# Kernel optimization log

Hardware: AMD Instinct MI355X
Metric: run time of the kernel (lower is better)

## Reference

```python
import jax, jax.numpy as jnp
import numpy as np

B, S, D, C_IN = 8, 1024, 512, 7
INNER = 2 * D              # mLSTM up-projection (proj_factor=2)
NH_M, DH_M = 4, INNER // 4 # mLSTM heads = n_heads//2
NH_S, DH_S = 8, D // 8     # sLSTM heads = n_heads
K_M, K_S = 7, 4            # conv kernels: enc_in, factor
FF = int(1.1 * D)          # sLSTM gated-FFN dim (proj_factor=1.1)
EPS = 1e-6
NEG = -1e30


def _ln(x, w):
    mu = x.mean(-1, keepdims=True)
    var = x.var(-1, keepdims=True)
    return (x - mu) * jax.lax.rsqrt(var + 1e-5) * w


def _headnorm(h, w):
    # h: [B,S,NH,DH] -> per-head groupnorm -> [B,S,NH*DH] * w
    mu = h.mean(-1, keepdims=True)
    var = h.var(-1, keepdims=True)
    hn = (h - mu) * jax.lax.rsqrt(var + 1e-5)
    b, s = h.shape[:2]
    return hn.reshape(b, s, -1) * w


def _causal_conv1d(x, w, b):
    # depthwise causal conv. x: [B,S,C], w: [C,k], b: [C]
    k = w.shape[1]
    xp = jnp.pad(x, ((0, 0), (k - 1, 0), (0, 0))).transpose(0, 2, 1)  # [B,C,S+k-1]
    y = jax.lax.conv_general_dilated(
        xp, w[:, None, :], (1,), 'VALID',
        dimension_numbers=('NCH', 'OIH', 'NCH'),
        feature_group_count=w.shape[0])
    return y.transpose(0, 2, 1) + b


def _mlstm_parallel(q, k, v, i_pre, f_pre):
    # q,k,v: [B,NH,S,DH]; i_pre,f_pre: [B,NH,S]. Stabilized parallel mLSTM cell.
    s = q.shape[2]
    logf = jax.nn.log_sigmoid(f_pre)
    cum = jnp.concatenate([jnp.zeros_like(logf[:, :, :1]), jnp.cumsum(logf, -1)], -1)  # [B,NH,S+1]
    dmat = cum[:, :, 1:, None] - cum[:, :, None, 1:]            # [B,NH,S,S]
    mask = jnp.tril(jnp.ones((s, s), bool))
    dmat = jnp.where(mask, dmat, NEG) + i_pre[:, :, None, :]    # add igate along keys
    m = dmat.max(-1, keepdims=True)                              # stabilizer
    Dm = jnp.exp(dmat - m)
    qk = jnp.einsum('bhqd,bhkd->bhqk', q, k) * (q.shape[-1] ** -0.5)
    C = qk * Dm
    n = jnp.maximum(jnp.abs(C.sum(-1, keepdims=True)), jnp.exp(-m)) + EPS
    return jnp.einsum('bhqk,bhkd->bhqd', C / n, v)               # [B,NH,S,DH]


def _forward(x_enc, x_mark_enc, x_dec, x_mark_dec, W_in, b_in,
             m_ln_w, m_Wup, m_bup, m_conv_w, m_conv_b, m_Wq, m_Wk, m_Wv,
             m_Wi, m_bi, m_Wf, m_bf, m_norm_w, m_skip, m_Wdown, m_bdown,
             s_ln_w, s_conv_w, s_conv_b, s_Wi, s_Wf, s_Wz, s_Wo,
             s_Ri, s_Rf, s_Rz, s_Ro, s_bi, s_bf, s_bz, s_bo, s_norm_w,
             s_ffn_ln_w, s_Wff_up, s_bff_up, s_Wff_down, s_bff_down,
             post_norm_w, W_out, b_out):
    b, s, _ = x_enc.shape
    x = x_enc @ W_in + b_in                                    # [B,S,D]

    # ---- block 0: mLSTM block ----
    res = x
    xn = _ln(x, m_ln_w)
    xm, z = jnp.split(xn @ m_Wup + m_bup, 2, axis=-1)          # each [B,S,INNER]
    conv = jax.nn.silu(_causal_conv1d(xm, m_conv_w, m_conv_b))
    qf, kf, vf = conv @ m_Wq, conv @ m_Wk, xm @ m_Wv
    gate_in = jnp.concatenate([qf, kf, vf], -1)                # [B,S,3*INNER]
    i_pre = (gate_in @ m_Wi + m_bi).transpose(0, 2, 1)         # [B,NH,S]
    f_pre = (gate_in @ m_Wf + m_bf).transpose(0, 2, 1)
    to_h = lambda t: t.reshape(b, s, NH_M, DH_M).transpose(0, 2, 1, 3)
    h = _mlstm_parallel(to_h(qf), to_h(kf), to_h(vf), i_pre, f_pre)
    h = h.transpose(0, 2, 1, 3)                                # [B,S,NH,DH]
    h = _headnorm(h, m_norm_w) + m_skip * conv                 # learnable skip
    x = res + (h * jax.nn.silu(z)) @ m_Wdown + m_bdown

    # ---- block 1: sLSTM block + gated FFN ----
    res = x
    xn = _ln(x, s_ln_w)
    conv = jax.nn.silu(_causal_conv1d(xn, s_conv_w, s_conv_b))
    gh = lambda t: t.reshape(b, s, NH_S, DH_S).transpose(1, 0, 2, 3)  # time-major
    gi, gf = gh(conv @ s_Wi + s_bi), gh(conv @ s_Wf + s_bf)
    gz, go = gh(xn @ s_Wz + s_bz), gh(xn @ s_Wo + s_bo)

    def step(carry, xs):
        c, n, m, hp = carry
        xi, xf, xz, xo = xs
        rec = lambda R: jnp.einsum('bhd,hde->bhe', hp, R)      # block-diag recurrent
        it, ft = xi + rec(s_Ri), xf + rec(s_Rf)
        zt, ot = xz + rec(s_Rz), xo + rec(s_Ro)
        m_new = jnp.maximum(ft + m, it)                        # exp-gate stabilizer
        ig = jnp.exp(it - m_new)
        fg = jnp.exp(ft + m - m_new)
        c_new = fg * c + ig * jnp.tanh(zt)
        n_new = fg * n + ig
        h_new = jax.nn.sigmoid(ot) * c_new / jnp.maximum(n_new, EPS)
        return (c_new, n_new, m_new, h_new), h_new

    z0 = jnp.zeros((b, NH_S, DH_S), x.dtype)
    _, hs = jax.lax.scan(step, (z0, z0, z0, z0), (gi, gf, gz, go))
    x = res + _headnorm(hs.transpose(1, 0, 2, 3), s_norm_w)

    res = x
    a, g = jnp.split(_ln(x, s_ffn_ln_w) @ s_Wff_up + s_bff_up, 2, axis=-1)
    x = res + (jax.nn.gelu(a) * g) @ s_Wff_down + s_bff_down

    x = _ln(x, post_norm_w)                                    # post-blocks norm
    return x @ W_out + b_out                                   # [B,S,7]


def setup_inputs() -> dict:
    key = jax.random.key(0)
    ks = iter(jax.random.split(key, 64))
    rn = lambda shape, sc=0.02: jax.random.normal(next(ks), shape, jnp.float32) * sc
    return {
        'x_enc': jax.random.normal(next(ks), (B, S, C_IN), jnp.float32),
        'x_mark_enc': jax.random.normal(next(ks), (B, S, 4), jnp.float32),
        'x_dec': jax.random.normal(next(ks), (B, S, C_IN), jnp.float32),
        'x_mark_dec': jax.random.normal(next(ks), (B, S, 4), jnp.float32),
        'W_in': rn((C_IN, D)), 'b_in': jnp.zeros((D,)),
        'm_ln_w': jnp.ones((D,)),
        'm_Wup': rn((D, 2 * INNER)), 'm_bup': jnp.zeros((2 * INNER,)),
        'm_conv_w': rn((INNER, K_M), 0.1), 'm_conv_b': jnp.zeros((INNER,)),
        'm_Wq': rn((INNER, INNER)), 'm_Wk': rn((INNER, INNER)), 'm_Wv': rn((INNER, INNER)),
        'm_Wi': rn((3 * INNER, NH_M)), 'm_bi': jnp.zeros((NH_M,)),
        'm_Wf': rn((3 * INNER, NH_M)), 'm_bf': jnp.full((NH_M,), 3.0),
        'm_norm_w': jnp.ones((INNER,)), 'm_skip': jnp.ones((INNER,)),
        'm_Wdown': rn((INNER, D)), 'm_bdown': jnp.zeros((D,)),
        's_ln_w': jnp.ones((D,)),
        's_conv_w': rn((D, K_S), 0.1), 's_conv_b': jnp.zeros((D,)),
        's_Wi': rn((D, D)), 's_Wf': rn((D, D)), 's_Wz': rn((D, D)), 's_Wo': rn((D, D)),
        's_Ri': rn((NH_S, DH_S, DH_S)), 's_Rf': rn((NH_S, DH_S, DH_S)),
        's_Rz': rn((NH_S, DH_S, DH_S)), 's_Ro': rn((NH_S, DH_S, DH_S)),
        's_bi': jnp.zeros((D,)), 's_bf': jnp.linspace(3.0, 6.0, D),
        's_bz': jnp.zeros((D,)), 's_bo': jnp.zeros((D,)),
        's_norm_w': jnp.ones((D,)),
        's_ffn_ln_w': jnp.ones((D,)),
        's_Wff_up': rn((D, 2 * FF)), 's_bff_up': jnp.zeros((2 * FF,)),
        's_Wff_down': rn((FF, D)), 's_bff_down': jnp.zeros((D,)),
        'post_norm_w': jnp.ones((D,)),
        'W_out': rn((D, C_IN)), 'b_out': jnp.zeros((C_IN,)),
    }


def reference(x_enc, x_mark_enc, x_dec, x_mark_dec, W_in, b_in,
              m_ln_w, m_Wup, m_bup, m_conv_w, m_conv_b, m_Wq, m_Wk, m_Wv,
              m_Wi, m_bi, m_Wf, m_bf, m_norm_w, m_skip, m_Wdown, m_bdown,
              s_ln_w, s_conv_w, s_conv_b, s_Wi, s_Wf, s_Wz, s_Wo,
              s_Ri, s_Rf, s_Rz, s_Ro, s_bi, s_bf, s_bz, s_bo, s_norm_w,
              s_ffn_ln_w, s_Wff_up, s_bff_up, s_Wff_down, s_bff_down,
              post_norm_w, W_out, b_out):
    return _forward(x_enc, x_mark_enc, x_dec, x_mark_dec, W_in, b_in,
                    m_ln_w, m_Wup, m_bup, m_conv_w, m_conv_b, m_Wq, m_Wk, m_Wv,
                    m_Wi, m_bi, m_Wf, m_bf, m_norm_w, m_skip, m_Wdown, m_bdown,
                    s_ln_w, s_conv_w, s_conv_b, s_Wi, s_Wf, s_Wz, s_Wo,
                    s_Ri, s_Rf, s_Rz, s_Ro, s_bi, s_bf, s_bz, s_bo, s_norm_w,
                    s_ffn_ln_w, s_Wff_up, s_bff_up, s_Wff_down, s_bff_down,
                    post_norm_w, W_out, b_out)
```

## Files before the change

### kernel.cpp

```cpp
#include <hip/hip_runtime.h>
#include <hip/hip_bf16.h>
#include <math.h>

typedef __hip_bfloat16 bf16;
typedef __attribute__((ext_vector_type(4))) float f32x4;
typedef __attribute__((ext_vector_type(8))) short bf16x8;
typedef __attribute__((ext_vector_type(8))) unsigned short u16x8;

#define DEV static __device__ __forceinline__

DEV float b2f(bf16 x) { return __bfloat162float(x); }
DEV bf16 f2b(float x) { return __float2bfloat16(x); }
DEV unsigned short f2us(float x) { bf16 h = __float2bfloat16(x); return *reinterpret_cast<unsigned short*>(&h); }
DEV float us2f(unsigned short u) { unsigned v = (unsigned)u << 16; float f; __builtin_memcpy(&f, &v, 4); return f; }

DEV float loadw(const void* p, size_t i, int bf) {
  return bf ? __bfloat162float(((const bf16*)p)[i]) : ((const float*)p)[i];
}

DEV float wredsum(float v) {
#pragma unroll
  for (int off = 32; off > 0; off >>= 1) v += __shfl_xor(v, off);
  return v;
}

DEV void gload_lds16(const void* g, void* l) {
  __builtin_amdgcn_global_load_lds((const __attribute__((address_space(1))) char*)g,
                                   (__attribute__((address_space(3))) char*)l, 16, 0, 0);
}

__global__ void k_flag(const unsigned* __restrict__ w1, int* flag) {
  if (threadIdx.x == 0 && blockIdx.x == 0) *flag = (*w1 == 0x3F800000u) ? 0 : 1;
}

__global__ void k_transpose(const void* __restrict__ W, int ldw, int colOff, bf16* __restrict__ Wt,
                            int K, int N, int Kpad, int Npad, const int* __restrict__ fp) {
  int bf = *fp;
  __shared__ float t[32][33];
  int n0 = blockIdx.x * 32, k0 = blockIdx.y * 32;
  int tx = threadIdx.x & 31, ty = threadIdx.x >> 5;
  for (int i = ty; i < 32; i += 8) {
    int k = k0 + i, n = n0 + tx;
    t[i][tx] = (k < K && n < N) ? loadw(W, (size_t)k * ldw + colOff + n, bf) : 0.f;
  }
  __syncthreads();
  for (int i = ty; i < 32; i += 8) {
    int n = n0 + i, k = k0 + tx;
    if (n < Npad && k < Kpad) Wt[(size_t)n * Kpad + k] = f2b(t[tx][i]);
  }
}

template <int MODE>
__global__ __launch_bounds__(256) void k_gemm(
    const bf16* __restrict__ A, int lda, const bf16* __restrict__ Bt, int ldb,
    bf16* __restrict__ Cout, int ldc, const bf16* __restrict__ Res,
    const void* __restrict__ bias, int biasOff, const void* __restrict__ bias2, int bias2Off,
    int colSplit, int Nreal, int K, const int* __restrict__ fp) {
  int bf = *fp;
  __shared__ bf16 As[128 * 32];
  __shared__ bf16 Bs[128 * 32];
  int tid = threadIdx.x, wv = tid >> 6, lane = tid & 63;
  int mBase = blockIdx.y * 128, nBase = blockIdx.x * 128;
  int wm = (wv & 1) * 64, wn = (wv >> 1) * 64;
  f32x4 acc[4][4];
#pragma unroll
  for (int i = 0; i < 4; i++)
#pragma unroll
    for (int j = 0; j < 4; j++) acc[i][j] = 0.f;
  int r0 = (wv * 2) * 16 + (lane >> 2);
  int r1 = (wv * 2 + 1) * 16 + (lane >> 2);
  int cc = (lane & 3) * 8;
  const bf16* a0 = A + (size_t)(mBase + r0) * lda + cc;
  const bf16* a1 = A + (size_t)(mBase + r1) * lda + cc;
  const bf16* b0 = Bt + (size_t)(nBase + r0) * ldb + cc;
  const bf16* b1 = Bt + (size_t)(nBase + r1) * ldb + cc;
  for (int kt = 0; kt < K; kt += 32) {
    __syncthreads();
    gload_lds16(a0 + kt, As + (wv * 2) * 512);
    gload_lds16(a1 + kt, As + (wv * 2 + 1) * 512);
    gload_lds16(b0 + kt, Bs + (wv * 2) * 512);
    gload_lds16(b1 + kt, Bs + (wv * 2 + 1) * 512);
    __syncthreads();
    bf16x8 af[4], bfr[4];
#pragma unroll
    for (int i = 0; i < 4; i++) {
      af[i] = *(const bf16x8*)(As + (wm + i * 16 + (lane & 15)) * 32 + (lane >> 4) * 8);
      bfr[i] = *(const bf16x8*)(Bs + (wn + i * 16 + (lane & 15)) * 32 + (lane >> 4) * 8);
    }
#pragma unroll
    for (int i = 0; i < 4; i++)
#pragma unroll
      for (int j = 0; j < 4; j++)
        acc[i][j] = __builtin_amdgcn_mfma_f32_16x16x32_bf16(af[i], bfr[j], acc[i][j], 0, 0, 0);
  }
#pragma unroll
  for (int i = 0; i < 4; i++) {
#pragma unroll
    for (int j = 0; j < 4; j++) {
      int n = nBase + wn + j * 16 + (lane & 15);
      if (n < Nreal) {
        float bv = 0.f;
        if (bias) bv = (n < colSplit) ? loadw(bias, biasOff + n, bf)
                                      : loadw(bias2, bias2Off + n - colSplit, bf);
#pragma unroll
        for (int r = 0; r < 4; r++) {
          int m = mBase + wm + i * 16 + (lane >> 4) * 4 + r;
          float v = acc[i][j][r] + bv;
          if (MODE == 1) v += b2f(Res[(size_t)m * 512 + n]);
          if (MODE == 2) {
            float yo = b2f(Cout[(size_t)m * ldc + n]);
            Cout[(size_t)m * ldc + n] = f2b(yo * (v / (1.f + __expf(-v))));
          } else {
            Cout[(size_t)m * ldc + n] = f2b(v);
          }
        }
      }
    }
  }
}

__global__ __launch_bounds__(256) void k_embed_ln(
    const void* __restrict__ xe, const void* __restrict__ Wi, const void* __restrict__ bi,
    const void* __restrict__ lw, bf16* __restrict__ x, bf16* __restrict__ xn,
    const int* __restrict__ fp) {
  int bf = *fp;
  int lane = threadIdx.x & 63, wv = threadIdx.x >> 6;
  size_t row = blockIdx.x * 4 + wv;
  float e[7];
#pragma unroll
  for (int c = 0; c < 7; c++) e[c] = loadw(xe, row * 7 + c, bf);
  float v[8];
#pragma unroll
  for (int j = 0; j < 8; j++) {
    int d = j * 64 + lane;
    float a = loadw(bi, d, bf);
#pragma unroll
    for (int c = 0; c < 7; c++) a += e[c] * loadw(Wi, c * 512 + d, bf);
    v[j] = a;
  }
  float s = 0, s2 = 0;
#pragma unroll
  for (int j = 0; j < 8; j++) { s += v[j]; s2 += v[j] * v[j]; }
  s = wredsum(s); s2 = wredsum(s2);
  float mu = s * (1.f / 512.f);
  float var = s2 * (1.f / 512.f) - mu * mu;
  float rq = rsqrtf(fmaxf(var, 0.f) + 1e-5f);
#pragma unroll
  for (int j = 0; j < 8; j++) {
    int d = j * 64 + lane;
    x[row * 512 + d] = f2b(v[j]);
    xn[row * 512 + d] = f2b((v[j] - mu) * rq * loadw(lw, d, bf));
  }
}

template <int KW>
__global__ void k_conv(const bf16* __restrict__ X, int ldx, int c4shift,
                       const void* __restrict__ cw, const void* __restrict__ cb,
                       bf16* __restrict__ out, int C, const int* __restrict__ fp) {
  int bf = *fp;
  int idx = blockIdx.x * 256 + threadIdx.x;
  int r = idx >> c4shift;
  int c4 = (idx & ((1 << c4shift) - 1)) * 4;
  int b = r >> 10, s = r & 1023;
  float a[4];
#pragma unroll
  for (int t = 0; t < 4; t++) a[t] = loadw(cb, c4 + t, bf);
#pragma unroll
  for (int j = 0; j < KW; j++) {
    int sj = s - (KW - 1) + j;
    if (sj >= 0) {
      const bf16* px = X + ((size_t)(b << 10) + sj) * ldx + c4;
#pragma unroll
      for (int t = 0; t < 4; t++) a[t] += b2f(px[t]) * loadw(cw, (c4 + t) * KW + j, bf);
    }
  }
#pragma unroll
  for (int t = 0; t < 4; t++) {
    float v = a[t];
    v = v / (1.f + __expf(-v));
    out[(size_t)r * C + c4 + t] = f2b(v);
  }
}

__global__ __launch_bounds__(256) void k_mgates(
    const bf16* __restrict__ qf, const bf16* __restrict__ kf, const bf16* __restrict__ vf,
    const void* __restrict__ Wi, const void* __restrict__ bi,
    const void* __restrict__ Wf, const void* __restrict__ bfv,
    float* __restrict__ ipre, float* __restrict__ fpre, const int* __restrict__ fp) {
  int bf = *fp;
  int lane = threadIdx.x & 63, wv = threadIdx.x >> 6;
  int row = blockIdx.x * 4 + wv;
  int b = row >> 10, s = row & 1023;
  float ai[4] = {0, 0, 0, 0}, af[4] = {0, 0, 0, 0};
  const bf16* srcs[3] = {qf + (size_t)row * 1024, kf + (size_t)row * 1024, vf + (size_t)row * 1024};
#pragma unroll
  for (int p = 0; p < 3; p++) {
    const bf16* sp = srcs[p];
#pragma unroll
    for (int it = 0; it < 16; it++) {
      int d = it * 64 + lane;
      float g = b2f(sp[d]);
      size_t wr = (size_t)(p * 1024 + d) * 4;
#pragma unroll
      for (int h = 0; h < 4; h++) {
        ai[h] += g * loadw(Wi, wr + h, bf);
        af[h] += g * loadw(Wf, wr + h, bf);
      }
    }
  }
#pragma unroll
  for (int h = 0; h < 4; h++) { ai[h] = wredsum(ai[h]); af[h] = wredsum(af[h]); }
  if (lane == 0) {
#pragma unroll
    for (int h = 0; h < 4; h++) {
      ipre[(size_t)(b * 4 + h) * 1024 + s] = ai[h] + loadw(bi, h, bf);
      fpre[(size_t)(b * 4 + h) * 1024 + s] = af[h] + loadw(bfv, h, bf);
    }
  }
}

__global__ void k_mprep(const float* __restrict__ ipre, const float* __restrict__ fpre,
                        float* __restrict__ aq, float* __restrict__ bk, float* __restrict__ bmax) {
  int bh = blockIdx.x, lane = threadIdx.x;
  float cum = 0.f, rmax = -3.4e38f;
  for (int t = 0; t < 1024; t += 64) {
    float f = fpre[(size_t)bh * 1024 + t + lane];
    float lf = fminf(f, 0.f) - log1pf(__expf(-fabsf(f)));
    float sc = lf;
#pragma unroll
    for (int off = 1; off < 64; off <<= 1) {
      float o = __shfl_up(sc, off);
      if (lane >= off) sc += o;
    }
    float a = cum + sc;
    float bkv = ipre[(size_t)bh * 1024 + t + lane] - a;
    float mx = bkv;
#pragma unroll
    for (int off = 1; off < 64; off <<= 1) {
      float o = __shfl_up(mx, off);
      if (lane >= off) mx = fmaxf(mx, o);
    }
    float m = fmaxf(rmax, mx);
    aq[(size_t)bh * 1024 + t + lane] = a;
    bk[(size_t)bh * 1024 + t + lane] = bkv;
    bmax[(size_t)bh * 1024 + t + lane] = m;
    cum += __shfl(sc, 63);
    rmax = fmaxf(rmax, __shfl(mx, 63));
  }
}

__global__ void k_vtrans(const bf16* __restrict__ vf, bf16* __restrict__ vt) {
  __shared__ bf16 t[32][33];
  int s0 = blockIdx.x * 32, d0 = blockIdx.y * 32, bh = blockIdx.z;
  int b = bh >> 2, h = bh & 3;
  int tx = threadIdx.x & 31, ty = threadIdx.x >> 5;
  for (int i = ty; i < 32; i += 8)
    t[i][tx] = vf[((size_t)(b << 10) + s0 + i) * 1024 + h * 256 + d0 + tx];
  __syncthreads();
  for (int i = ty; i < 32; i += 8)
    vt[((size_t)bh * 256 + d0 + i) * 1024 + s0 + tx] = t[tx][i];
}

__global__ __launch_bounds__(256) void k_mlstm(
    const bf16* __restrict__ qf, const bf16* __restrict__ kf, const bf16* __restrict__ vt,
    const float* __restrict__ aq, const float* __restrict__ bk, const float* __restrict__ bmax,
    const bf16* __restrict__ conv, const void* __restrict__ nw, const void* __restrict__ skip,
    bf16* __restrict__ y, const int* __restrict__ fp) {
  int bf = *fp;
  __shared__ bf16 Ks[64 * 256];
  __shared__ bf16 Vs[256 * 64];
  __shared__ unsigned short Ps[4][1024];
  int qt = blockIdx.x, bh = blockIdx.y;
  int b = bh >> 2, h = bh & 3;
  int tid = threadIdx.x, wv = tid >> 6, lane = tid & 63;
  size_t rowbase = (size_t)b << 10;
  int qw = qt * 64 + wv * 16;
  bf16x8 qreg[8];
  {
    const bf16* qp = qf + (rowbase + qw + (lane & 15)) * 1024 + h * 256 + (lane >> 4) * 8;
#pragma unroll
    for (int ck = 0; ck < 8; ck++) qreg[ck] = *(const bf16x8*)(qp + ck * 32);
  }
  float bmq[4], aqv[4];
#pragma unroll
  for (int r = 0; r < 4; r++) {
    int qg = qw + (lane >> 4) * 4 + r;
    bmq[r] = bmax[(size_t)bh * 1024 + qg];
    aqv[r] = aq[(size_t)bh * 1024 + qg];
  }
  f32x4 oacc[16];
#pragma unroll
  for (int i = 0; i < 16; i++) oacc[i] = 0.f;
  float rs[4] = {0, 0, 0, 0};
  int nkt = qt + 1;
  for (int kt = 0; kt < nkt; kt++) {
    int kbase = kt * 64;
    __syncthreads();
#pragma unroll
    for (int j = 0; j < 8; j++) {
      int ch = wv * 8 + j;
      int krow = ch * 2 + (lane >> 5);
      int sunit = (lane & 31) ^ (krow & 7);
      gload_lds16(kf + (rowbase + kbase + krow) * 1024 + h * 256 + sunit * 8, Ks + ch * 512);
    }
#pragma unroll
    for (int j = 0; j < 8; j++) {
      int ch = wv * 8 + j;
      int drow = ch * 8 + (lane >> 3);
      int sunit = (lane & 7) ^ (drow & 7);
      gload_lds16(vt + ((size_t)bh * 256 + drow) * 1024 + kbase + sunit * 8, Vs + ch * 512);
    }
    __syncthreads();
    float bkl = bk[(size_t)bh * 1024 + kbase + lane];
    f32x4 sacc[4];
#pragma unroll
    for (int kfg = 0; kfg < 4; kfg++) {
      int krow = kfg * 16 + (lane & 15);
      const char* kp = (const char*)Ks + krow * 512;
      int swz = (krow & 7) << 4;
      f32x4 sa = 0.f;
#pragma unroll
      for (int ck = 0; ck < 8; ck++) {
        int cb = (ck * 32 + (lane >> 4) * 8) * 2;
        bf16x8 bb = *(const bf16x8*)(kp + (cb ^ swz));
        sa = __builtin_amdgcn_mfma_f32_16x16x32_bf16(qreg[ck], bb, sa, 0, 0, 0);
      }
      sacc[kfg] = sa;
    }
    int qr0 = (lane >> 4) * 4;
#pragma unroll
    for (int kfg = 0; kfg < 4; kfg++) {
      int kloc = kfg * 16 + (lane & 15);
      float bkv = __shfl(bkl, kloc);
      int kglob = kbase + kloc;
#pragma unroll
      for (int r = 0; r < 4; r++) {
        int qloc = qr0 + r;
        int qglob = qt * 64 + wv * 16 + qloc;
        float p = sacc[kfg][r] * 0.0625f * __expf(bkv - bmq[r]);
        if (kglob > qglob) p = 0.f;
        rs[r] += p;
        int boff = qloc * 128 + ((kloc * 2) ^ ((qloc & 7) << 4));
        Ps[wv][boff >> 1] = f2us(p);
      }
    }
    __syncthreads();
#pragma unroll
    for (int kc = 0; kc < 2; kc++) {
      int qloc = lane & 15;
      int pboff = qloc * 128 + (((kc * 32 + (lane >> 4) * 8) * 2) ^ ((qloc & 7) << 4));
      bf16x8 pa = *(const bf16x8*)((const char*)Ps[wv] + pboff);
#pragma unroll
      for (int nf = 0; nf < 16; nf++) {
        int dr = nf * 16 + (lane & 15);
        int vboff = dr * 128 + (((kc * 32 + (lane >> 4) * 8) * 2) ^ ((dr & 7) << 4));
        bf16x8 vb = *(const bf16x8*)((const char*)Vs + vboff);
        oacc[nf] = __builtin_amdgcn_mfma_f32_16x16x32_bf16(pa, vb, oacc[nf], 0, 0, 0);
      }
    }
  }
#pragma unroll
  for (int r = 0; r < 4; r++) {
#pragma unroll
    for (int off = 1; off < 16; off <<= 1) rs[r] += __shfl_xor(rs[r], off);
  }
  float invn[4], mu[4], rqv[4];
#pragma unroll
  for (int r = 0; r < 4; r++) {
    float m = aqv[r] + bmq[r];
    float n = fmaxf(fabsf(rs[r]), __expf(-m)) + 1e-6f;
    invn[r] = 1.f / n;
  }
#pragma unroll
  for (int r = 0; r < 4; r++) {
    float s = 0.f, s2 = 0.f;
#pragma unroll
    for (int nf = 0; nf < 16; nf++) {
      float x = oacc[nf][r] * invn[r];
      s += x; s2 += x * x;
    }
#pragma unroll
    for (int off = 1; off < 16; off <<= 1) { s += __shfl_xor(s, off); s2 += __shfl_xor(s2, off); }
    mu[r] = s * (1.f / 256.f);
    float var = s2 * (1.f / 256.f) - mu[r] * mu[r];
    rqv[r] = rsqrtf(fmaxf(var, 0.f) + 1e-5f);
  }
#pragma unroll
  for (int nf = 0; nf < 16; nf++) {
    int dcol = h * 256 + nf * 16 + (lane & 15);
    float nwv = loadw(nw, dcol, bf);
    float skv = loadw(skip, dcol, bf);
#pragma unroll
    for (int r = 0; r < 4; r++) {
      size_t row = rowbase + qw + (lane >> 4) * 4 + r;
      float hn = (oacc[nf][r] * invn[r] - mu[r]) * rqv[r];
      float cv = b2f(conv[row * 1024 + dcol]);
      y[row * 1024 + dcol] = f2b(hn * nwv + skv * cv);
    }
  }
}

__global__ __launch_bounds__(256) void k_ln512(const bf16* __restrict__ X,
                                               const void* __restrict__ w,
                                               bf16* __restrict__ out,
                                               const int* __restrict__ fp) {
  int bf = *fp;
  int lane = threadIdx.x & 63, wv = threadIdx.x >> 6;
  size_t row = blockIdx.x * 4 + wv;
  float v[8];
  u16x8 q = *(const u16x8*)(X + row * 512 + lane * 8);
#pragma unroll
  for (int t = 0; t < 8; t++) v[t] = us2f(q[t]);
  float s = 0, s2 = 0;
#pragma unroll
  for (int t = 0; t < 8; t++) { s += v[t]; s2 += v[t] * v[t]; }
  s = wredsum(s); s2 = wredsum(s2);
  float mu = s * (1.f / 512.f), var = s2 * (1.f / 512.f) - mu * mu;
  float rq = rsqrtf(fmaxf(var, 0.f) + 1e-5f);
#pragma unroll
  for (int t = 0; t < 8; t++) {
    int d = lane * 8 + t;
    out[row * 512 + d] = f2b((v[t] - mu) * rq * loadw(w, d, bf));
  }
}

__global__ __launch_bounds__(256) void k_scan(
    const bf16* __restrict__ gif, const bf16* __restrict__ gzo,
    const void* __restrict__ Ri, const void* __restrict__ Rf,
    const void* __restrict__ Rz, const void* __restrict__ Ro,
    float* __restrict__ hs, const int* __restrict__ fp) {
  int bf = *fp;
  __shared__ __align__(16) float hbuf[2][64];
  int blk = blockIdx.x, b = blk >> 3, h = blk & 7;
  int w = threadIdx.x >> 6, lane = threadIdx.x & 63;
  int e_loc = lane & 15, d_blk = lane >> 4;
  int e = w * 16 + e_loc;
  int d0 = d_blk * 16;
  float Rg[4][16];
  const void* Rp[4] = {Ri, Rf, Rz, Ro};
#pragma unroll
  for (int g = 0; g < 4; g++)
#pragma unroll
    for (int d = 0; d < 16; d++)
      Rg[g][d] = loadw(Rp[g], (size_t)h * 4096 + (size_t)(d0 + d) * 64 + e, bf);
  size_t base = ((size_t)b << 10) * 1024 + h * 64 + e;
  size_t hsbase = (((size_t)b << 10)) * 512 + h * 64 + e;
  float c = 0.f, n = 0.f, m = 0.f;
  if (threadIdx.x < 64) { hbuf[0][threadIdx.x] = 0.f; hbuf[1][threadIdx.x] = 0.f; }
  __syncthreads();
  float xi = b2f(gif[base]), xf = b2f(gif[base + 512]);
  float xz = b2f(gzo[base]), xo = b2f(gzo[base + 512]);
  int p = 0;
  for (int s = 0; s < 1024; s++) {
    float hv[16];
#pragma unroll
    for (int t = 0; t < 16; t += 4) {
      f32x4 q = *(const f32x4*)(&hbuf[p][d0 + t]);
      hv[t] = q[0]; hv[t + 1] = q[1]; hv[t + 2] = q[2]; hv[t + 3] = q[3];
    }
    float ci = xi, cf = xf, cz = xz, co = xo;
    float a[4] = {0.f, 0.f, 0.f, 0.f};
    if (s < 1023) {
      size_t nb = base + (size_t)(s + 1) * 1024;
      xi = b2f(gif[nb]); xf = b2f(gif[nb + 512]);
      xz = b2f(gzo[nb]); xo = b2f(gzo[nb + 512]);
    }
#pragma unroll
    for (int g = 0; g < 4; g++) {
      float p0 = 0, p1 = 0, p2 = 0, p3 = 0;
#pragma unroll
      for (int d = 0; d < 16; d += 4) {
        p0 += hv[d] * Rg[g][d];
        p1 += hv[d + 1] * Rg[g][d + 1];
        p2 += hv[d + 2] * Rg[g][d + 2];
        p3 += hv[d + 3] * Rg[g][d + 3];
      }
      a[g] += (p0 + p1) + (p2 + p3);
    }
#pragma unroll
    for (int g = 0; g < 4; g++) {
      a[g] += __shfl_xor(a[g], 16);
      a[g] += __shfl_xor(a[g], 32);
    }
    float it = a[0] + ci, ft = a[1] + cf, zt = a[2] + cz, ot = a[3] + co;
    float mn = fmaxf(ft + m, it);
    float ig = __expf(it - mn);
    float fg = __expf(ft + m - mn);
    float tz = 1.f - 2.f / (__expf(2.f * zt) + 1.f);
    c = fg * c + ig * tz;
    n = fg * n + ig;
    m = mn;
    float hvn = (1.f / (1.f + __expf(-ot))) * c / fmaxf(n, 1e-6f);
    if (d_blk == 0) hbuf[p ^ 1][e] = hvn;
    if (d_blk == 1) hs[hsbase + (size_t)s * 512] = hvn;
    p ^= 1;
    __syncthreads();
  }
}

__global__ __launch_bounds__(256) void k_snorm_ln(
    const bf16* __restrict__ x2, const float* __restrict__ hs, const void* __restrict__ nw,
    bf16* __restrict__ x3, const void* __restrict__ fw, bf16* __restrict__ xn3,
    const int* __restrict__ fp) {
  int bf = *fp;
  int lane = threadIdx.x & 63, wv = threadIdx.x >> 6;
  size_t row = blockIdx.x * 4 + wv;
  float v[8];
#pragma unroll
  for (int t = 0; t < 8; t += 4) {
    f32x4 q = *(const f32x4*)(hs + row * 512 + lane * 8 + t);
    v[t] = q[0]; v[t + 1] = q[1]; v[t + 2] = q[2]; v[t + 3] = q[3];
  }
  float s = 0, s2 = 0;
#pragma unroll
  for (int t = 0; t < 8; t++) { s += v[t]; s2 += v[t] * v[t]; }
#pragma unroll
  for (int off = 1; off < 8; off <<= 1) { s += __shfl_xor(s, off); s2 += __shfl_xor(s2, off); }
  float mu = s * (1.f / 64.f), var = s2 * (1.f / 64.f) - mu * mu;
  float rq = rsqrtf(fmaxf(var, 0.f) + 1e-5f);
  u16x8 qx = *(const u16x8*)(x2 + row * 512 + lane * 8);
  float xv[8];
  float ss = 0, ss2 = 0;
#pragma unroll
  for (int t = 0; t < 8; t++) {
    int d = lane * 8 + t;
    float val = us2f(qx[t]) + (v[t] - mu) * rq * loadw(nw, d, bf);
    xv[t] = val;
    x3[row * 512 + d] = f2b(val);
    ss += val; ss2 += val * val;
  }
  ss = wredsum(ss); ss2 = wredsum(ss2);
  float mu2 = ss * (1.f / 512.f), var2 = ss2 * (1.f / 512.f) - mu2 * mu2;
  float rq2 = rsqrtf(fmaxf(var2, 0.f) + 1e-5f);
#pragma unroll
  for (int t = 0; t < 8; t++) {
    int d = lane * 8 + t;
    xn3[row * 512 + d] = f2b((xv[t] - mu2) * rq2 * loadw(fw, d, bf));
  }
}

__global__ void k_gelugate(const bf16* __restrict__ comb, bf16* __restrict__ y2) {
  int idx = blockIdx.x * 256 + threadIdx.x;
  int r = idx / 576, j = idx - r * 576;
  float v = 0.f;
  if (j < 563) {
    float av = b2f(comb[(size_t)r * 1280 + j]);
    float gv = b2f(comb[(size_t)r * 1280 + 640 + j]);
    float u = 0.7978845608028654f * (av + 0.044715f * av * av * av);
    float th = 1.f - 2.f / (__expf(2.f * u) + 1.f);
    v = 0.5f * av * (1.f + th) * gv;
  }
  y2[(size_t)r * 576 + j] = f2b(v);
}

__global__ __launch_bounds__(256) void k_final(
    const bf16* __restrict__ x4, const void* __restrict__ pw,
    const void* __restrict__ Wo, const void* __restrict__ bo, void* __restrict__ out,
    const int* __restrict__ fp) {
  int bf = *fp;
  int lane = threadIdx.x & 63, wv = threadIdx.x >> 6;
  size_t row = blockIdx.x * 4 + wv;
  float v[8];
  u16x8 q = *(const u16x8*)(x4 + row * 512 + lane * 8);
#pragma unroll
  for (int t = 0; t < 8; t++) v[t] = us2f(q[t]);
  float s = 0, s2 = 0;
#pragma unroll
  for (int t = 0; t < 8; t++) { s += v[t]; s2 += v[t] * v[t]; }
  s = wredsum(s); s2 = wredsum(s2);
  float mu = s * (1.f / 512.f), var = s2 * (1.f / 512.f) - mu * mu;
  float rq = rsqrtf(fmaxf(var, 0.f) + 1e-5f);
  float o[7] = {0, 0, 0, 0, 0, 0, 0};
#pragma unroll
  for (int t = 0; t < 8; t++) {
    int d = lane * 8 + t;
    float xn = (v[t] - mu) * rq * loadw(pw, d, bf);
#pragma unroll
    for (int cc = 0; cc < 7; cc++) o[cc] += xn * loadw(Wo, d * 7 + cc, bf);
  }
#pragma unroll
  for (int cc = 0; cc < 7; cc++) o[cc] = wredsum(o[cc]);
  if (lane == 0) {
#pragma unroll
    for (int cc = 0; cc < 7; cc++) {
      float r = o[cc] + loadw(bo, cc, bf);
      if (bf) ((bf16*)out)[row * 7 + cc] = f2b(r);
      else ((float*)out)[row * 7 + cc] = r;
    }
  }
}

extern "C" void kernel_launch(void* const* d_in, const int* in_sizes, int n_in,
                              void* d_out, int out_size, void* d_ws, size_t ws_size,
                              hipStream_t stream) {
  const void* x_enc = d_in[0];
  const void* W_in = d_in[4];
  const void* b_in = d_in[5];
  const void* m_ln_w = d_in[6];
  const void* m_Wup = d_in[7];
  const void* m_bup = d_in[8];
  const void* m_conv_w = d_in[9];
  const void* m_conv_b = d_in[10];
  const void* m_Wq = d_in[11];
  const void* m_Wk = d_in[12];
  const void* m_Wv = d_in[13];
  const void* m_Wi = d_in[14];
  const void* m_bi = d_in[15];
  const void* m_Wf = d_in[16];
  const void* m_bf = d_in[17];
  const void* m_norm_w = d_in[18];
  const void* m_skip = d_in[19];
  const void* m_Wdown = d_in[20];
  const void* m_bdown = d_in[21];
  const void* s_ln_w = d_in[22];
  const void* s_conv_w = d_in[23];
  const void* s_conv_b = d_in[24];
  const void* s_Wi = d_in[25];
  const void* s_Wf = d_in[26];
  const void* s_Wz = d_in[27];
  const void* s_Wo = d_in[28];
  const void* s_Ri = d_in[29];
  const void* s_Rf = d_in[30];
  const void* s_Rz = d_in[31];
  const void* s_Ro = d_in[32];
  const void* s_bi = d_in[33];
  const void* s_bf = d_in[34];
  const void* s_bz = d_in[35];
  const void* s_bo = d_in[36];
  const void* s_norm_w = d_in[37];
  const void* s_ffn_ln_w = d_in[38];
  const void* s_Wff_up = d_in[39];
  const void* s_bff_up = d_in[40];
  const void* s_Wff_down = d_in[41];
  const void* s_bff_down = d_in[42];
  const void* post_norm_w = d_in[43];
  const void* W_out = d_in[44];
  const void* b_out = d_in[45];

  char* ws = (char*)d_ws;
  size_t off = 0;
  auto alloc = [&](size_t bytes) { void* p = ws + off; off += (bytes + 255) & ~(size_t)255; return p; };
  const size_t M = 8192;
  const int BIG = 1 << 30;

  int* flag = (int*)alloc(256);
  float* ipre = (float*)alloc(32 * 1024 * 4);
  float* fpre = (float*)alloc(32 * 1024 * 4);
  float* aqB = (float*)alloc(32 * 1024 * 4);
  float* bkB = (float*)alloc(32 * 1024 * 4);
  float* bmB = (float*)alloc(32 * 1024 * 4);
  bf16* R1 = (bf16*)alloc(M * 512 * 2);
  bf16* R2 = (bf16*)alloc(M * 512 * 2);
  bf16* T1 = (bf16*)alloc(M * 512 * 2);
  bf16* SA = (bf16*)alloc(M * 1024 * 2);
  bf16* SB = (bf16*)alloc(M * 1024 * 2);
  bf16* SC = (bf16*)alloc(M * 1024 * 2);
  bf16* SD = (bf16*)alloc(M * 1024 * 2);
  bf16* SE = (bf16*)alloc(M * 1024 * 2);
  bf16* ARENA = (bf16*)alloc((size_t)8 * 1024 * 1024);
  (void)ws_size;

  bf16* wt_up = ARENA;
  bf16* wt_q = ARENA + (size_t)2048 * 512;
  bf16* wt_k = wt_q + (size_t)1024 * 1024;
  bf16* wt_v = wt_k + (size_t)1024 * 1024;
  bf16* wt_down = ARENA;
  bf16* wt_i = ARENA + (size_t)512 * 1024;
  bf16* wt_f = wt_i + (size_t)512 * 512;
  bf16* wt_z = wt_f + (size_t)512 * 512;
  bf16* wt_o = wt_z + (size_t)512 * 512;
  bf16* wt_ffa = ARENA;
  bf16* wt_ffg = wt_ffa + (size_t)640 * 512;
  bf16* wt_ffdn = wt_ffg + (size_t)640 * 512;

  k_flag<<<1, 64, 0, stream>>>((const unsigned*)m_ln_w, flag);

  k_transpose<<<dim3(64, 16), 256, 0, stream>>>(m_Wup, 2048, 0, wt_up, 512, 2048, 512, 2048, flag);
  k_transpose<<<dim3(32, 32), 256, 0, stream>>>(m_Wq, 1024, 0, wt_q, 1024, 1024, 1024, 1024, flag);
  k_transpose<<<dim3(32, 32), 256, 0, stream>>>(m_Wk, 1024, 0, wt_k, 1024, 1024, 1024, 1024, flag);
  k_transpose<<<dim3(32, 32), 256, 0, stream>>>(m_Wv, 1024, 0, wt_v, 1024, 1024, 1024, 1024, flag);

  k_embed_ln<<<2048, 256, 0, stream>>>(x_enc, W_in, b_in, m_ln_w, R1, T1, flag);
  k_gemm<0><<<dim3(8, 64), 256, 0, stream>>>(T1, 512, wt_up, 512, SA, 1024, nullptr, m_bup, 0, nullptr, 0, BIG, 1024, 512, flag);
  k_conv<7><<<8192, 256, 0, stream>>>(SA, 1024, 8, m_conv_w, m_conv_b, SB, 1024, flag);
  k_gemm<0><<<dim3(8, 64), 256, 0, stream>>>(SB, 1024, wt_q, 1024, SC, 1024, nullptr, nullptr, 0, nullptr, 0, BIG, 1024, 1024, flag);
  k_gemm<0><<<dim3(8, 64), 256, 0, stream>>>(SB, 1024, wt_k, 1024, SD, 1024, nullptr, nullptr, 0, nullptr, 0, BIG, 1024, 1024, flag);
  k_gemm<0><<<dim3(8, 64), 256, 0, stream>>>(SA, 1024, wt_v, 1024, SE, 1024, nullptr, nullptr, 0, nullptr, 0, BIG, 1024, 1024, flag);
  k_mgates<<<2048, 256, 0, stream>>>(SC, SD, SE, m_Wi, m_bi, m_Wf, m_bf, ipre, fpre, flag);
  k_mprep<<<32, 64, 0, stream>>>(ipre, fpre, aqB, bkB, bmB);
  bf16* vt = SA;
  k_vtrans<<<dim3(32, 8, 32), 256, 0, stream>>>(SE, vt);
  k_mlstm<<<dim3(16, 32), 256, 0, stream>>>(SC, SD, vt, aqB, bkB, bmB, SB, m_norm_w, m_skip, SB, flag);
  k_gemm<2><<<dim3(8, 64), 256, 0, stream>>>(T1, 512, wt_up + (size_t)1024 * 512, 512, SB, 1024, nullptr, m_bup, 1024, nullptr, 0, BIG, 1024, 512, flag);
  k_transpose<<<dim3(16, 32), 256, 0, stream>>>(m_Wdown, 512, 0, wt_down, 1024, 512, 1024, 512, flag);
  k_transpose<<<dim3(16, 16), 256, 0, stream>>>(s_Wi, 512, 0, wt_i, 512, 512, 512, 512, flag);
  k_transpose<<<dim3(16, 16), 256, 0, stream>>>(s_Wf, 512, 0, wt_f, 512, 512, 512, 512, flag);
  k_transpose<<<dim3(16, 16), 256, 0, stream>>>(s_Wz, 512, 0, wt_z, 512, 512, 512, 512, flag);
  k_transpose<<<dim3(16, 16), 256, 0, stream>>>(s_Wo, 512, 0, wt_o, 512, 512, 512, 512, flag);
  k_gemm<1><<<dim3(4, 64), 256, 0, stream>>>(SB, 1024, wt_down, 1024, R2, 512, R1, m_bdown, 0, nullptr, 0, BIG, 512, 1024, flag);

  k_ln512<<<2048, 256, 0, stream>>>(R2, s_ln_w, T1, flag);
  k_conv<4><<<4096, 256, 0, stream>>>(T1, 512, 7, s_conv_w, s_conv_b, SE, 512, flag);
  k_gemm<0><<<dim3(8, 64), 256, 0, stream>>>(SE, 512, wt_i, 512, SA, 1024, nullptr, s_bi, 0, s_bf, 0, 512, 1024, 512, flag);
  k_gemm<0><<<dim3(8, 64), 256, 0, stream>>>(T1, 512, wt_z, 512, SC, 1024, nullptr, s_bz, 0, s_bo, 0, 512, 1024, 512, flag);
  k_transpose<<<dim3(20, 16), 256, 0, stream>>>(s_Wff_up, 1126, 0, wt_ffa, 512, 563, 512, 640, flag);
  k_transpose<<<dim3(20, 16), 256, 0, stream>>>(s_Wff_up, 1126, 563, wt_ffg, 512, 563, 512, 640, flag);
  k_transpose<<<dim3(16, 18), 256, 0, stream>>>(s_Wff_down, 512, 0, wt_ffdn, 563, 512, 576, 512, flag);
  float* hsF = (float*)SD;
  k_scan<<<64, 256, 0, stream>>>(SA, SC, s_Ri, s_Rf, s_Rz, s_Ro, hsF, flag);
  k_snorm_ln<<<2048, 256, 0, stream>>>(R2, hsF, s_norm_w, R1, s_ffn_ln_w, T1, flag);

  k_gemm<0><<<dim3(10, 64), 256, 0, stream>>>(T1, 512, wt_ffa, 512, SA, 1280, nullptr, s_bff_up, 0, s_bff_up, 563, 640, 1203, 512, flag);
  bf16* y2 = SD;
  k_gelugate<<<18432, 256, 0, stream>>>(SA, y2);
  k_gemm<1><<<dim3(4, 64), 256, 0, stream>>>(y2, 576, wt_ffdn, 576, R2, 512, R1, s_bff_down, 0, nullptr, 0, BIG, 512, 576, flag);

  k_final<<<2048, 256, 0, stream>>>(R2, post_norm_w, W_out, b_out, d_out, flag);
}
```

Measured before the change: 1.631 ms.

## Run sLSTM recurrent scan in a single wavefront using readlane broadcasts

The sLSTM scan now runs each (batch, head) recurrence with one 64-lane wavefront instead of four. Each lane holds all 64 recurrent weights per gate (256 registers), and the previous hidden state is broadcast with readlane instead of going through an LDS double buffer. This removes the per-step __syncthreads and the cross-lane shuffle reductions that sat on the serial critical path. The cost is four times more FMAs per lane per step, very high register pressure, and 64 serial readlanes per step, which can lengthen the dependent chain.

```diff
diff --git a/kernel.cpp b/kernel.cpp
--- a/kernel.cpp
+++ b/kernel.cpp
@@ -22,6 +22,13 @@
 #pragma unroll
   for (int off = 32; off > 0; off >>= 1) v += __shfl_xor(v, off);
   return v;
+}
+
+DEV float rdlane(float v, int l) {
+  unsigned u; __builtin_memcpy(&u, &v, 4);
+  unsigned r = __builtin_amdgcn_readlane(u, l);
+  float f; __builtin_memcpy(&f, &r, 4);
+  return f;
 }
 
 DEV void gload_lds16(const void* g, void* l) {
@@ -424,65 +431,52 @@
   }
 }
 
-__global__ __launch_bounds__(256) void k_scan(
+__global__ __launch_bounds__(64, 1) void k_scan(
     const bf16* __restrict__ gif, const bf16* __restrict__ gzo,
     const void* __restrict__ Ri, const void* __restrict__ Rf,
     const void* __restrict__ Rz, const void* __restrict__ Ro,
     float* __restrict__ hs, const int* __restrict__ fp) {
   int bf = *fp;
-  __shared__ __align__(16) float hbuf[2][64];
   int blk = blockIdx.x, b = blk >> 3, h = blk & 7;
-  int w = threadIdx.x >> 6, lane = threadIdx.x & 63;
-  int e_loc = lane & 15, d_blk = lane >> 4;
-  int e = w * 16 + e_loc;
-  int d0 = d_blk * 16;
-  float Rg[4][16];
+  int e = threadIdx.x;
+  float Rg[4][64];
   const void* Rp[4] = {Ri, Rf, Rz, Ro};
 #pragma unroll
   for (int g = 0; g < 4; g++)
 #pragma unroll
-    for (int d = 0; d < 16; d++)
-      Rg[g][d] = loadw(Rp[g], (size_t)h * 4096 + (size_t)(d0 + d) * 64 + e, bf);
+    for (int d = 0; d < 64; d++)
+      Rg[g][d] = loadw(Rp[g], (size_t)h * 4096 + (size_t)d * 64 + e, bf);
   size_t base = ((size_t)b << 10) * 1024 + h * 64 + e;
-  size_t hsbase = (((size_t)b << 10)) * 512 + h * 64 + e;
-  float c = 0.f, n = 0.f, m = 0.f;
-  if (threadIdx.x < 64) { hbuf[0][threadIdx.x] = 0.f; hbuf[1][threadIdx.x] = 0.f; }
-  __syncthreads();
+  size_t hsbase = ((size_t)b << 10) * 512 + h * 64 + e;
+  float c = 0.f, n = 0.f, m = 0.f, hcur = 0.f;
   float xi = b2f(gif[base]), xf = b2f(gif[base + 512]);
   float xz = b2f(gzo[base]), xo = b2f(gzo[base + 512]);
-  int p = 0;
   for (int s = 0; s < 1024; s++) {
-    float hv[16];
-#pragma unroll
-    for (int t = 0; t < 16; t += 4) {
-      f32x4 q = *(const f32x4*)(&hbuf[p][d0 + t]);
-      hv[t] = q[0]; hv[t + 1] = q[1]; hv[t + 2] = q[2]; hv[t + 3] = q[3];
-    }
     float ci = xi, cf = xf, cz = xz, co = xo;
-    float a[4] = {0.f, 0.f, 0.f, 0.f};
     if (s < 1023) {
       size_t nb = base + (size_t)(s + 1) * 1024;
       xi = b2f(gif[nb]); xf = b2f(gif[nb + 512]);
       xz = b2f(gzo[nb]); xo = b2f(gzo[nb + 512]);
     }
-#pragma unroll
-    for (int g = 0; g < 4; g++) {
-      float p0 = 0, p1 = 0, p2 = 0, p3 = 0;
-#pragma unroll
-      for (int d = 0; d < 16; d += 4) {
-        p0 += hv[d] * Rg[g][d];
-        p1 += hv[d + 1] * Rg[g][d + 1];
-        p2 += hv[d + 2] * Rg[g][d + 2];
-        p3 += hv[d + 3] * Rg[g][d + 3];
+    float p0[4] = {0, 0, 0, 0}, p1[4] = {0, 0, 0, 0}, p2[4] = {0, 0, 0, 0}, p3[4] = {0, 0, 0, 0};
+#pragma unroll
+    for (int d = 0; d < 64; d += 4) {
+      float h0 = rdlane(hcur, d);
+      float h1 = rdlane(hcur, d + 1);
+      float h2 = rdlane(hcur, d + 2);
+      float h3 = rdlane(hcur, d + 3);
+#pragma unroll
+      for (int g = 0; g < 4; g++) {
+        p0[g] += h0 * Rg[g][d];
+        p1[g] += h1 * Rg[g][d + 1];
+        p2[g] += h2 * Rg[g][d + 2];
+        p3[g] += h3 * Rg[g][d + 3];
       }
-      a[g] += (p0 + p1) + (p2 + p3);
-    }
-#pragma unroll
-    for (int g = 0; g < 4; g++) {
-      a[g] += __shfl_xor(a[g], 16);
-      a[g] += __shfl_xor(a[g], 32);
-    }
-    float it = a[0] + ci, ft = a[1] + cf, zt = a[2] + cz, ot = a[3] + co;
+    }
+    float it = ci + (p0[0] + p1[0]) + (p2[0] + p3[0]);
+    float ft = cf + (p0[1] + p1[1]) + (p2[1] + p3[1]);
+    float zt = cz + (p0[2] + p1[2]) + (p2[2] + p3[2]);
+    float ot = co + (p0[3] + p1[3]) + (p2[3] + p3[3]);
     float mn = fmaxf(ft + m, it);
     float ig = __expf(it - mn);
     float fg = __expf(ft + m - mn);
@@ -490,11 +484,8 @@
     c = fg * c + ig * tz;
     n = fg * n + ig;
     m = mn;
-    float hvn = (1.f / (1.f + __expf(-ot))) * c / fmaxf(n, 1e-6f);
-    if (d_blk == 0) hbuf[p ^ 1][e] = hvn;
-    if (d_blk == 1) hs[hsbase + (size_t)s * 512] = hvn;
-    p ^= 1;
-    __syncthreads();
+    hcur = (1.f / (1.f + __expf(-ot))) * c / fmaxf(n, 1e-6f);
+    hs[hsbase + (size_t)s * 512] = hcur;
   }
 }
 
@@ -707,7 +698,7 @@
   k_transpose<<<dim3(20, 16), 256, 0, stream>>>(s_Wff_up, 1126, 563, wt_ffg, 512, 563, 512, 640, flag);
   k_transpose<<<dim3(16, 18), 256, 0, stream>>>(s_Wff_down, 512, 0, wt_ffdn, 563, 512, 576, 512, flag);
   float* hsF = (float*)SD;
-  k_scan<<<64, 256, 0, stream>>>(SA, SC, s_Ri, s_Rf, s_Rz, s_Ro, hsF, flag);
+  k_scan<<<64, 64, 0, stream>>>(SA, SC, s_Ri, s_Rf, s_Rz, s_Ro, hsF, flag);
   k_snorm_ln<<<2048, 256, 0, stream>>>(R2, hsF, s_norm_w, R1, s_ffn_ln_w, T1, flag);
 
   k_gemm<0><<<dim3(10, 64), 256, 0, stream>>>(T1, 512, wt_ffa, 512, SA, 1280, nullptr, s_bff_up, 0, s_bff_up, 563, 640, 1203, 512, flag);
```

After: 1.944 ms. 19.2% more time.
